# Kernel tuning notes

Measured on AMD Instinct MI355X. Metric: run time of the kernel, lower is better.

The kernel has to match this reference:

```python
import jax, jax.numpy as jnp
import numpy as np

D_KEY, BANK_N = 128, 9720
BS, N = 1, 1620          # n = h*w = 30*54 (480p features, stride 16)
D_VAL, C, OBJ_N = 512, 512, 3


def setup_inputs() -> dict:
    key = jax.random.key(0)
    k1, k2, k3, k4, k5 = jax.random.split(key, 5)
    return {
        "keys_bank": jax.random.normal(k1, (D_KEY, BANK_N), dtype=jnp.float32),
        "q_in": jax.random.normal(k2, (BS, D_KEY, N), dtype=jnp.float32),
        "q_out": jax.random.normal(k3, (OBJ_N, C, N), dtype=jnp.float32),
        "values": jax.random.normal(k4, (OBJ_N, D_VAL, BANK_N), dtype=jnp.float32),
        "masks": jax.random.uniform(k5, (OBJ_N, 1, BANK_N), dtype=jnp.float32),
    }


def reference(keys_bank, q_in, q_out, values, masks):
    # p[b,k,n] = softmax_k( keys^T q_in / sqrt(d_key) )
    d_key = keys_bank.shape[0]
    scale = 1.0 / np.sqrt(d_key).astype(np.float32)
    p = jnp.einsum("dk,bdn->bkn", keys_bank, q_in) * scale
    p = jax.nn.softmax(p, axis=1)  # over bank dim

    # Batched over objects (original loops per object, sharing p)
    mem = jnp.einsum("ovk,bkn->obvn", values, p)       # (obj, bs, d_val, n)
    mask_mem = jnp.einsum("ouk,bkn->obun", masks, p)   # (obj, bs, 1, n)
    q_out_with_mask = q_out[:, None, :, :] * mask_mem  # (obj, bs, C, n)

    out = jnp.concatenate([mem, q_out_with_mask], axis=2)  # (obj, bs, d_val+C, n)
    return jnp.swapaxes(out, 0, 1)                          # (bs, obj, d_val+C, n)
```

## Files before the change

### kernel.cpp

```cpp
#include <hip/hip_runtime.h>
#include <hip/hip_bf16.h>

typedef unsigned short u16;
typedef unsigned char  u8;

#define D_KEY   128
#define BANK_N  9720
#define BANK_P  9728
#define N_TOK   1620
#define N_PAD   1664
#define OBJ_N   3
#define M_PAD   1664
#define LDCOL   1664
#define ONES_ROW 1539
#define QK_SCALE 0.08838834764831845f

typedef __bf16 bf16x8 __attribute__((ext_vector_type(8)));
typedef float  f32x4  __attribute__((ext_vector_type(4)));
typedef unsigned int u32x4 __attribute__((ext_vector_type(4)));
typedef int i32x8 __attribute__((ext_vector_type(8)));

__device__ __forceinline__ float bf2f(u16 u) {
  union { unsigned int i; float f; } v; v.i = ((unsigned int)u) << 16; return v.f;
}
__device__ __forceinline__ u16 f2bf(float f) {
  unsigned int x = __float_as_uint(f);
  unsigned int r = x + 0x7fffu + ((x >> 16) & 1u);
  return (u16)(r >> 16);
}
__device__ __forceinline__ unsigned pack_fp8x4(float a, float b, float c, float d) {
  unsigned v = __builtin_amdgcn_cvt_pk_fp8_f32(a, b, 0, false);
  v = __builtin_amdgcn_cvt_pk_fp8_f32(c, d, v, true);
  return v;
}
__device__ __forceinline__ u8 f2fp8(float a) {
  return (u8)(__builtin_amdgcn_cvt_pk_fp8_f32(a, 0.f, 0, false) & 0xff);
}

__device__ __forceinline__ void load_lds16(const void* g, void* l) {
  __builtin_amdgcn_global_load_lds(
      (const __attribute__((address_space(1))) void*)g,
      (__attribute__((address_space(3))) void*)l, 16, 0, 0);
}

__global__ void prep(const float* __restrict__ q, const float* __restrict__ keys,
                     const float* __restrict__ values, const float* __restrict__ masks,
                     u16* __restrict__ qT, u16* __restrict__ kT, u8* __restrict__ vm8) {
  __shared__ float t[64][65];
  int b = blockIdx.x;
  if (b < 832) {
    int idx = b * 256 + threadIdx.x;
    int n = idx >> 7, d = idx & 127;
    float v = (n < N_TOK) ? q[d * N_TOK + n] * QK_SCALE : 0.f;
    qT[idx] = f2bf(v);
    return;
  }
  if (b < 1136) {
    b -= 832;
    const int bk = (b % 152) * 64;
    const int bd = (b / 152) * 64;
    const int tx = threadIdx.x & 63;
    const int ty = threadIdx.x >> 6;
#pragma unroll
    for (int i = 0; i < 64; i += 4) {
      int d = bd + ty + i;
      int k = bk + tx;
      t[ty + i][tx] = (k < BANK_N) ? keys[(size_t)d * BANK_N + k] : 0.f;
    }
    __syncthreads();
#pragma unroll
    for (int i = 0; i < 64; i += 4) {
      int r = ty + i;
      kT[(size_t)(bk + r) * D_KEY + bd + tx] = f2bf(t[tx][r]);
    }
    return;
  }
  const int NV = BANK_P / 4;
  int idx = (b - 1136) * 256 + threadIdx.x;
  if (idx >= M_PAD * NV) return;
  int m = idx / NV;
  int k4 = (idx - m * NV) * 4;
  float4 v = make_float4(0.f, 0.f, 0.f, 0.f);
  if (m == ONES_ROW) {
    v.x = (k4     < BANK_N) ? 1.f : 0.f;
    v.y = (k4 + 1 < BANK_N) ? 1.f : 0.f;
    v.z = (k4 + 2 < BANK_N) ? 1.f : 0.f;
    v.w = (k4 + 3 < BANK_N) ? 1.f : 0.f;
  } else {
    const float* src = nullptr;
    if (m < 1536)          src = values + (size_t)m * BANK_N;
    else if (m < ONES_ROW) src = masks + (size_t)(m - 1536) * BANK_N;
    if (src) {
      if (k4 + 3 < BANK_N) v = *(const float4*)(src + k4);
      else {
        if (k4     < BANK_N) v.x = src[k4];
        if (k4 + 1 < BANK_N) v.y = src[k4 + 1];
        if (k4 + 2 < BANK_N) v.z = src[k4 + 2];
        if (k4 + 3 < BANK_N) v.w = src[k4 + 3];
      }
    }
  }
  *(unsigned*)(vm8 + (size_t)m * BANK_P + k4) = pack_fp8x4(v.x, v.y, v.z, v.w);
}

__global__ void gemm_qk(const u16* __restrict__ A, const u16* __restrict__ B,
                        u8* __restrict__ E8)
{
  __shared__ __align__(16) u16 sbuf[8192];
  u16* As = sbuf;
  u16* Bs = sbuf + 4096;

  const int tid  = threadIdx.x;
  const int wave = tid >> 6;
  const int lane = tid & 63;
  const int bn = blockIdx.x % 76, bm = blockIdx.x / 76;

  const u16* Abase = A + (size_t)bm * 128 * D_KEY;
  const u16* Bbase = B + (size_t)bn * 128 * D_KEY;

  const int r  = lane >> 2;
  const int c8 = (lane & 3) << 3;
  const int s0 = wave, s1 = wave + 4;

  f32x4 acc[4][4];
#pragma unroll
  for (int i = 0; i < 4; i++)
#pragma unroll
    for (int j = 0; j < 4; j++) acc[i][j] = (f32x4){0.f, 0.f, 0.f, 0.f};

  const int m_in = lane & 15;
  const int quad = lane >> 4;
  const int wm = (wave >> 1) * 64;
  const int wn = (wave & 1) * 64;

  for (int kt = 0; kt < D_KEY; kt += 32) {
    load_lds16(Abase + (size_t)(s0 * 16 + r) * D_KEY + kt + c8, &As[s0 * 512]);
    load_lds16(Abase + (size_t)(s1 * 16 + r) * D_KEY + kt + c8, &As[s1 * 512]);
    load_lds16(Bbase + (size_t)(s0 * 16 + r) * D_KEY + kt + c8, &Bs[s0 * 512]);
    load_lds16(Bbase + (size_t)(s1 * 16 + r) * D_KEY + kt + c8, &Bs[s1 * 512]);
    __syncthreads();

    bf16x8 af[4], bfr[4];
#pragma unroll
    for (int i = 0; i < 4; i++)
      af[i] = *(const bf16x8*)&As[(wm + i * 16 + m_in) * 32 + quad * 8];
#pragma unroll
    for (int j = 0; j < 4; j++)
      bfr[j] = *(const bf16x8*)&Bs[(wn + j * 16 + m_in) * 32 + quad * 8];
#pragma unroll
    for (int i = 0; i < 4; i++)
#pragma unroll
      for (int j = 0; j < 4; j++)
        acc[i][j] = __builtin_amdgcn_mfma_f32_16x16x32_bf16(af[i], bfr[j], acc[i][j], 0, 0, 0);
    __syncthreads();
  }

  u8* sb8 = (u8*)sbuf;
#pragma unroll
  for (int i = 0; i < 4; i++)
#pragma unroll
    for (int j = 0; j < 4; j++)
#pragma unroll
      for (int t = 0; t < 4; t++) {
        int row_l = wm + i * 16 + quad * 4 + t;
        int col_l = wn + j * 16 + m_in;
        bool valid = (bn * 128 + col_l) < BANK_N;
        sb8[(row_l << 7) + col_l] = valid ? f2fp8(__expf(acc[i][j][t])) : (u8)0;
      }
  __syncthreads();

  for (int chunk = tid; chunk < 1024; chunk += 256) {
    int row = chunk >> 3;
    int cu  = (chunk & 7) << 4;
    u32x4 v = *(const u32x4*)&sb8[(row << 7) + cu];
    *(u32x4*)&E8[(size_t)(bm * 128 + row) * BANK_P + bn * 128 + cu] = v;
  }
}

__global__ __launch_bounds__(256, 3)
void gemm_pv(const u8* __restrict__ A, const u8* __restrict__ B,
             u16* __restrict__ memC, int kChunk, size_t cPartStride)
{
  __shared__ __align__(16) u16 sbuf[16384];
  u8* As8 = (u8*)sbuf;
  u8* Bs8 = (u8*)sbuf + 16384;

  const int tid  = threadIdx.x;
  const int wave = tid >> 6;
  const int lane = tid & 63;

  int b = blockIdx.x;
  int bz = b / 169;
  int rr = b - bz * 169;
  int gid = rr / 52;
  int rem = rr - gid * 52;
  int width = (gid < 3) ? 4 : 1;
  int bm = rem / width;
  int bn = gid * 4 + (rem - bm * width);

  const int kbeg = bz * kChunk;
  const int kend = kbeg + kChunk;

  const u8* Abase = A + (size_t)bm * 128 * BANK_P;
  const u8* Bbase = B + (size_t)bn * 128 * BANK_P;

  const int srow  = lane >> 1;
  const int shalf = (((lane & 1) ^ ((lane >> 3) & 1)) << 4);

  f32x4 acc[4][4];
#pragma unroll
  for (int i = 0; i < 4; i++)
#pragma unroll
    for (int j = 0; j < 4; j++) acc[i][j] = (f32x4){0.f, 0.f, 0.f, 0.f};

  const int m_in = lane & 15;
  const int quad = lane >> 4;
  const int wm = (wave >> 1) * 64;
  const int wn = (wave & 1) * 64;
  const int fxor = ((m_in >> 2) & 1) << 4;

  const size_t arow_off = (size_t)(wave * 32 + srow) * BANK_P;

  for (int kt = kbeg; kt < kend; kt += 128) {
#pragma unroll
    for (int s = 0; s < 4; s++)
      load_lds16(Abase + arow_off + kt + s * 32 + shalf, As8 + s * 4096 + wave * 1024);
#pragma unroll
    for (int s = 0; s < 4; s++)
      load_lds16(Bbase + arow_off + kt + s * 32 + shalf, Bs8 + s * 4096 + wave * 1024);
    __syncthreads();

    i32x8 a8[4];
#pragma unroll
    for (int i = 0; i < 4; i++) {
      const u8* p = As8 + quad * 4096 + (wm + i * 16 + m_in) * 32;
      u32x4 lo = *(const u32x4*)(p + fxor);
      u32x4 hi = *(const u32x4*)(p + (fxor ^ 16));
      a8[i] = (i32x8){(int)lo[0], (int)lo[1], (int)lo[2], (int)lo[3],
                      (int)hi[0], (int)hi[1], (int)hi[2], (int)hi[3]};
    }
#pragma unroll
    for (int j = 0; j < 4; j++) {
      const u8* p = Bs8 + quad * 4096 + (wn + j * 16 + m_in) * 32;
      u32x4 lo = *(const u32x4*)(p + fxor);
      u32x4 hi = *(const u32x4*)(p + (fxor ^ 16));
      i32x8 b8 = (i32x8){(int)lo[0], (int)lo[1], (int)lo[2], (int)lo[3],
                         (int)hi[0], (int)hi[1], (int)hi[2], (int)hi[3]};
#pragma unroll
      for (int i = 0; i < 4; i++)
        acc[i][j] = __builtin_amdgcn_mfma_scale_f32_16x16x128_f8f6f4(
            a8[i], b8, acc[i][j], 0, 0,
            0, 0x7f7f7f7f, 0, 0x7f7f7f7f);
    }
    __syncthreads();
  }

  u16* Cg = memC + (size_t)bz * cPartStride;
#pragma unroll
  for (int h = 0; h < 2; h++) {
    __syncthreads();
    if ((wave >> 1) == h) {
#pragma unroll
      for (int i = 0; i < 4; i++)
#pragma unroll
        for (int j = 0; j < 4; j++)
#pragma unroll
          for (int t = 0; t < 4; t++) {
            int row_l = i * 16 + quad * 4 + t;
            int col_l = wn + j * 16 + m_in;
            sbuf[(row_l << 7) + col_l] = f2bf(acc[i][j][t]);
          }
    }
    __syncthreads();
    for (int chunk = tid; chunk < 1024; chunk += 256) {
      int row = chunk >> 4;
      int cu  = (chunk & 15) << 3;
      u32x4 v = *(const u32x4*)&sbuf[(row << 7) + cu];
      __builtin_nontemporal_store(
          v, (u32x4*)&Cg[(size_t)(bm * 128 + h * 64 + row) * LDCOL + bn * 128 + cu]);
    }
  }
}

__global__ void epilogue(const u16* __restrict__ memC, const float* __restrict__ q_out,
                         float* __restrict__ out, int nParts) {
  const int NV = N_TOK / 4;
  int idx = blockIdx.x * 256 + threadIdx.x;
  if (idx >= OBJ_N * 1024 * NV) return;
  int n4 = (idx % NV) * 4;
  int t = idx / NV;
  int c = t & 1023;
  int o = t >> 10;
  const size_t ps = (size_t)M_PAD * LDCOL;

  const u16* lbase = memC + (size_t)ONES_ROW * LDCOL + n4;
  float4 l = make_float4(0.f, 0.f, 0.f, 0.f);
  for (int z = 0; z < nParts; z++) {
    ushort4 v = *(const ushort4*)(lbase + z * ps);
    l.x += bf2f(v.x); l.y += bf2f(v.y); l.z += bf2f(v.z); l.w += bf2f(v.w);
  }

  size_t rowoff = (c < 512) ? (size_t)(o * 512 + c) * LDCOL
                            : (size_t)(1536 + o) * LDCOL;
  const u16* base = memC + rowoff + n4;
  float4 s = make_float4(0.f, 0.f, 0.f, 0.f);
  for (int z = 0; z < nParts; z++) {
    ushort4 v = *(const ushort4*)(base + z * ps);
    s.x += bf2f(v.x); s.y += bf2f(v.y); s.z += bf2f(v.z); s.w += bf2f(v.w);
  }
  float4 rv;
  float ix = 1.f / l.x, iy = 1.f / l.y, iz = 1.f / l.z, iw = 1.f / l.w;
  if (c < 512) {
    rv.x = s.x * ix; rv.y = s.y * iy; rv.z = s.z * iz; rv.w = s.w * iw;
  } else {
    float4 q = *(const float4*)(q_out + (size_t)(o * 512 + (c - 512)) * N_TOK + n4);
    rv.x = q.x * s.x * ix; rv.y = q.y * s.y * iy;
    rv.z = q.z * s.z * iz; rv.w = q.w * s.w * iw;
  }
  *(float4*)(out + (size_t)(o * 1024 + c) * N_TOK + n4) = rv;
}

extern "C" void kernel_launch(void* const* d_in, const int* in_sizes, int n_in,
                              void* d_out, int out_size, void* d_ws, size_t ws_size,
                              hipStream_t stream) {
  const float* keys   = (const float*)d_in[0];
  const float* q_in   = (const float*)d_in[1];
  const float* q_out  = (const float*)d_in[2];
  const float* values = (const float*)d_in[3];
  const float* masks  = (const float*)d_in[4];
  float* out = (float*)d_out;

  char* ws = (char*)d_ws;
  size_t off = 0;
  auto alloc = [&](size_t bytes) -> void* {
    void* p = ws + off; off += (bytes + 255) & ~(size_t)255; return p;
  };
  u16* qT  = (u16*)alloc((size_t)N_PAD * D_KEY * 2);
  u16* kT  = (u16*)alloc((size_t)BANK_P * D_KEY * 2);
  u8*  vm8 = (u8*)alloc((size_t)M_PAD * BANK_P);
  u8*  E8  = (u8*)alloc((size_t)N_PAD * BANK_P);

  int nParts = 4;
  while (nParts > 1 && off + (size_t)nParts * M_PAD * LDCOL * 2 > ws_size) nParts >>= 1;
  u16* memC = (u16*)alloc((size_t)nParts * M_PAD * LDCOL * 2);

  const int vmBlocks = (M_PAD * (BANK_P / 4) + 255) / 256;
  prep<<<1136 + vmBlocks, 256, 0, stream>>>(q_in, keys, values, masks, qT, kT, vm8);

  gemm_qk<<<988, 256, 0, stream>>>(qT, kT, E8);

  int kChunk = BANK_P / nParts;
  gemm_pv<<<dim3(169 * nParts), 256, 0, stream>>>(vm8, E8, memC, kChunk, (size_t)M_PAD * LDCOL);

  epilogue<<<(OBJ_N * 1024 * (N_TOK / 4) + 255) / 256, 256, 0, stream>>>(
      memC, q_out, out, nParts);
}
```

Measured before the change: 192.4 us.

## Double-buffer LDS staging in fp8 PV GEMM and remap blocks across XCDs

Doubles the gemm_pv shared buffer so the next K-tile's global-to-LDS loads are issued before the MFMAs on the current tile, with one explicit vmcnt wait and barrier per iteration in place of two syncthreads. It also remaps blockIdx so consecutive logical tiles land on the same XCD, which should improve L2 reuse of the shared A/B rows. The larger LDS footprint lowers the launch-bounds occupancy hint from 3 to 2 blocks per CU, so less latency hiding comes from other resident waves.

```diff
diff --git a/kernel.cpp b/kernel.cpp
--- a/kernel.cpp
+++ b/kernel.cpp
@@ -177,19 +177,22 @@
   }
 }
 
-__global__ __launch_bounds__(256, 3)
+__global__ __launch_bounds__(256, 2)
 void gemm_pv(const u8* __restrict__ A, const u8* __restrict__ B,
              u16* __restrict__ memC, int kChunk, size_t cPartStride)
 {
-  __shared__ __align__(16) u16 sbuf[16384];
-  u8* As8 = (u8*)sbuf;
-  u8* Bs8 = (u8*)sbuf + 16384;
+  __shared__ __align__(16) u16 sbuf[32768];
 
   const int tid  = threadIdx.x;
   const int wave = tid >> 6;
   const int lane = tid & 63;
 
-  int b = blockIdx.x;
+  const int nwg = 169 * (int)gridDim.x / 169 * 1;
+  const int bq = (int)gridDim.x >> 3, br = (int)gridDim.x & 7;
+  const int xcd = blockIdx.x & 7, bj = blockIdx.x >> 3;
+  int b = (xcd < br ? xcd * (bq + 1) : br * (bq + 1) + (xcd - br) * bq) + bj;
+  (void)nwg;
+
   int bz = b / 169;
   int rr = b - bz * 169;
   int gid = rr / 52;
@@ -199,13 +202,16 @@
   int bn = gid * 4 + (rem - bm * width);
 
   const int kbeg = bz * kChunk;
-  const int kend = kbeg + kChunk;
+  const int nt = kChunk >> 7;
 
   const u8* Abase = A + (size_t)bm * 128 * BANK_P;
   const u8* Bbase = B + (size_t)bn * 128 * BANK_P;
 
   const int srow  = lane >> 1;
   const int shalf = (((lane & 1) ^ ((lane >> 3) & 1)) << 4);
+  const size_t arow_off = (size_t)(wave * 32 + srow) * BANK_P;
+
+  u8* const lds0 = (u8*)sbuf;
 
   f32x4 acc[4][4];
 #pragma unroll
@@ -219,16 +225,28 @@
   const int wn = (wave & 1) * 64;
   const int fxor = ((m_in >> 2) & 1) << 4;
 
-  const size_t arow_off = (size_t)(wave * 32 + srow) * BANK_P;
-
-  for (int kt = kbeg; kt < kend; kt += 128) {
+  auto stagebuf = [&](int q, int kt) {
+    u8* As8_ = lds0 + q * 32768;
+    u8* Bs8_ = As8_ + 16384;
 #pragma unroll
     for (int s = 0; s < 4; s++)
-      load_lds16(Abase + arow_off + kt + s * 32 + shalf, As8 + s * 4096 + wave * 1024);
+      load_lds16(Abase + arow_off + kt + s * 32 + shalf, As8_ + s * 4096 + wave * 1024);
 #pragma unroll
     for (int s = 0; s < 4; s++)
-      load_lds16(Bbase + arow_off + kt + s * 32 + shalf, Bs8 + s * 4096 + wave * 1024);
-    __syncthreads();
+      load_lds16(Bbase + arow_off + kt + s * 32 + shalf, Bs8_ + s * 4096 + wave * 1024);
+  };
+
+  stagebuf(0, kbeg);
+  asm volatile("s_waitcnt vmcnt(0)" ::: "memory");
+  __builtin_amdgcn_s_barrier();
+  asm volatile("" ::: "memory");
+
+  for (int t = 0; t < nt; ++t) {
+    const int cur = t & 1;
+    if (t + 1 < nt) stagebuf(cur ^ 1, kbeg + (t + 1) * 128);
+
+    const u8* As8 = lds0 + cur * 32768;
+    const u8* Bs8 = As8 + 16384;
 
     i32x8 a8[4];
 #pragma unroll
@@ -252,7 +270,10 @@
             a8[i], b8, acc[i][j], 0, 0,
             0, 0x7f7f7f7f, 0, 0x7f7f7f7f);
     }
-    __syncthreads();
+
+    asm volatile("s_waitcnt vmcnt(0)" ::: "memory");
+    __builtin_amdgcn_s_barrier();
+    asm volatile("" ::: "memory");
   }
 
   u16* Cg = memC + (size_t)bz * cPartStride;
```

Result: no change. 192.6 us (+0.1%).

## Load PV GEMM fragments directly from global with register double-buffering

Applied to the files above, without the earlier changes.

The fp8 PV GEMM no longer stages A/B tiles through LDS with per-tile barriers. Each lane loads its MFMA fragments straight from global memory into registers, ping-ponging between two register sets so the next k-tile's loads overlap the current MFMAs. Block indices are also remapped so that consecutive logical blocks land on the same XCD for L2 locality. LDS shrinks and launch bounds drop to 2 blocks per CU to make room for the extra registers, at the cost of less coalesced global reads, no sharing of loaded data across waves (each tile is fetched twice), and lower occupancy.

```diff
diff --git a/kernel.cpp b/kernel.cpp
--- a/kernel.cpp
+++ b/kernel.cpp
@@ -177,19 +177,38 @@
   }
 }
 
-__global__ __launch_bounds__(256, 3)
+__device__ __forceinline__ i32x8 ldfrag(const u8* p) {
+  u32x4 lo = *(const u32x4*)p;
+  u32x4 hi = *(const u32x4*)(p + 16);
+  return (i32x8){(int)lo[0], (int)lo[1], (int)lo[2], (int)lo[3],
+                 (int)hi[0], (int)hi[1], (int)hi[2], (int)hi[3]};
+}
+
+__device__ __forceinline__ void mfmaset(const i32x8 (&aF)[4], const i32x8 (&bF)[4],
+                                        f32x4 (&acc)[4][4]) {
+#pragma unroll
+  for (int j = 0; j < 4; j++)
+#pragma unroll
+    for (int i = 0; i < 4; i++)
+      acc[i][j] = __builtin_amdgcn_mfma_scale_f32_16x16x128_f8f6f4(
+          aF[i], bF[j], acc[i][j], 0, 0,
+          0, 0x7f7f7f7f, 0, 0x7f7f7f7f);
+}
+
+__global__ __launch_bounds__(256, 2)
 void gemm_pv(const u8* __restrict__ A, const u8* __restrict__ B,
              u16* __restrict__ memC, int kChunk, size_t cPartStride)
 {
-  __shared__ __align__(16) u16 sbuf[16384];
-  u8* As8 = (u8*)sbuf;
-  u8* Bs8 = (u8*)sbuf + 16384;
+  __shared__ __align__(16) u16 sbuf[8192];
 
   const int tid  = threadIdx.x;
   const int wave = tid >> 6;
   const int lane = tid & 63;
 
-  int b = blockIdx.x;
+  const int bq = (int)gridDim.x >> 3, br = (int)gridDim.x & 7;
+  const int xcd = blockIdx.x & 7, bj = blockIdx.x >> 3;
+  int b = (xcd < br ? xcd * (bq + 1) : br * (bq + 1) + (xcd - br) * bq) + bj;
+
   int bz = b / 169;
   int rr = b - bz * 169;
   int gid = rr / 52;
@@ -199,76 +218,65 @@
   int bn = gid * 4 + (rem - bm * width);
 
   const int kbeg = bz * kChunk;
-  const int kend = kbeg + kChunk;
-
-  const u8* Abase = A + (size_t)bm * 128 * BANK_P;
-  const u8* Bbase = B + (size_t)bn * 128 * BANK_P;
-
-  const int srow  = lane >> 1;
-  const int shalf = (((lane & 1) ^ ((lane >> 3) & 1)) << 4);
-
-  f32x4 acc[4][4];
-#pragma unroll
-  for (int i = 0; i < 4; i++)
-#pragma unroll
-    for (int j = 0; j < 4; j++) acc[i][j] = (f32x4){0.f, 0.f, 0.f, 0.f};
+  const int nt = kChunk >> 7;
 
   const int m_in = lane & 15;
   const int quad = lane >> 4;
   const int wm = (wave >> 1) * 64;
   const int wn = (wave & 1) * 64;
-  const int fxor = ((m_in >> 2) & 1) << 4;
-
-  const size_t arow_off = (size_t)(wave * 32 + srow) * BANK_P;
-
-  for (int kt = kbeg; kt < kend; kt += 128) {
-#pragma unroll
-    for (int s = 0; s < 4; s++)
-      load_lds16(Abase + arow_off + kt + s * 32 + shalf, As8 + s * 4096 + wave * 1024);
-#pragma unroll
-    for (int s = 0; s < 4; s++)
-      load_lds16(Bbase + arow_off + kt + s * 32 + shalf, Bs8 + s * 4096 + wave * 1024);
-    __syncthreads();
-
-    i32x8 a8[4];
-#pragma unroll
-    for (int i = 0; i < 4; i++) {
-      const u8* p = As8 + quad * 4096 + (wm + i * 16 + m_in) * 32;
-      u32x4 lo = *(const u32x4*)(p + fxor);
-      u32x4 hi = *(const u32x4*)(p + (fxor ^ 16));
-      a8[i] = (i32x8){(int)lo[0], (int)lo[1], (int)lo[2], (int)lo[3],
-                      (int)hi[0], (int)hi[1], (int)hi[2], (int)hi[3]};
-    }
-#pragma unroll
-    for (int j = 0; j < 4; j++) {
-      const u8* p = Bs8 + quad * 4096 + (wn + j * 16 + m_in) * 32;
-      u32x4 lo = *(const u32x4*)(p + fxor);
-      u32x4 hi = *(const u32x4*)(p + (fxor ^ 16));
-      i32x8 b8 = (i32x8){(int)lo[0], (int)lo[1], (int)lo[2], (int)lo[3],
-                         (int)hi[0], (int)hi[1], (int)hi[2], (int)hi[3]};
+
+  const u8* pa[4];
+  const u8* pb[4];
+#pragma unroll
+  for (int i = 0; i < 4; i++) {
+    pa[i] = A + (size_t)(bm * 128 + wm + i * 16 + m_in) * BANK_P + kbeg + quad * 32;
+    pb[i] = B + (size_t)(bn * 128 + wn + i * 16 + m_in) * BANK_P + kbeg + quad * 32;
+  }
+
+  f32x4 acc[4][4];
+#pragma unroll
+  for (int i = 0; i < 4; i++)
+#pragma unroll
+    for (int j = 0; j < 4; j++) acc[i][j] = (f32x4){0.f, 0.f, 0.f, 0.f};
+
+  i32x8 aX[4], bX[4], aY[4], bY[4];
+#pragma unroll
+  for (int i = 0; i < 4; i++) { aX[i] = ldfrag(pa[i]); bX[i] = ldfrag(pb[i]); }
+
+  int t = 0;
+  for (; t + 2 < nt; t += 2) {
+#pragma unroll
+    for (int i = 0; i < 4; i++) { aY[i] = ldfrag(pa[i] + 128); bY[i] = ldfrag(pb[i] + 128); }
+    mfmaset(aX, bX, acc);
+#pragma unroll
+    for (int i = 0; i < 4; i++) { pa[i] += 256; pb[i] += 256; }
+#pragma unroll
+    for (int i = 0; i < 4; i++) { aX[i] = ldfrag(pa[i]); bX[i] = ldfrag(pb[i]); }
+    mfmaset(aY, bY, acc);
+  }
+  if (nt - t == 2) {
+#pragma unroll
+    for (int i = 0; i < 4; i++) { aY[i] = ldfrag(pa[i] + 128); bY[i] = ldfrag(pb[i] + 128); }
+    mfmaset(aX, bX, acc);
+    mfmaset(aY, bY, acc);
+  } else {
+    mfmaset(aX, bX, acc);
+  }
+
+  u16* Cg = memC + (size_t)bz * cPartStride;
+#pragma unroll
+  for (int h = 0; h < 2; h++) {
+    __syncthreads();
+    if ((wave >> 1) == h) {
 #pragma unroll
       for (int i = 0; i < 4; i++)
-        acc[i][j] = __builtin_amdgcn_mfma_scale_f32_16x16x128_f8f6f4(
-            a8[i], b8, acc[i][j], 0, 0,
-            0, 0x7f7f7f7f, 0, 0x7f7f7f7f);
-    }
-    __syncthreads();
-  }
-
-  u16* Cg = memC + (size_t)bz * cPartStride;
-#pragma unroll
-  for (int h = 0; h < 2; h++) {
-    __syncthreads();
-    if ((wave >> 1) == h) {
-#pragma unroll
-      for (int i = 0; i < 4; i++)
 #pragma unroll
         for (int j = 0; j < 4; j++)
 #pragma unroll
-          for (int t = 0; t < 4; t++) {
-            int row_l = i * 16 + quad * 4 + t;
+          for (int t4 = 0; t4 < 4; t4++) {
+            int row_l = i * 16 + quad * 4 + t4;
             int col_l = wn + j * 16 + m_in;
-            sbuf[(row_l << 7) + col_l] = f2bf(acc[i][j][t]);
+            sbuf[(row_l << 7) + col_l] = f2bf(acc[i][j][t4]);
           }
     }
     __syncthreads();
```

New measurement: 245.7 us. 27.7% more time.
